# Kernel tuning notes

Hardware: AMD Instinct MI355X
Metric: run time of the kernel (lower is better)

The kernel has to match this reference:

```python
import jax, jax.numpy as jnp
import numpy as np

K = 51           # kernel_size
DENSE_INNER = 2
EPS_LN = 1e-6
EPS_GRN = 1e-6

def _make_peripheral_coords(radius, dense_inner=2):
    coords = list(range(0, min(radius, dense_inner) + 1))
    v = 1
    while v < radius:
        v *= 2
        if v > dense_inner and v < radius:
            coords.append(v)
    if radius not in coords:
        coords.append(radius)
    return sorted(set(coords))

def _quantise(a, coords):
    q = 0
    for c in coords:
        if c <= a:
            q = c
        else:
            break
    return q

def _build_idx_map(kernel_size, dense_inner):
    radius = kernel_size // 2
    coords = _make_peripheral_coords(radius, dense_inner)
    signed = [-c for c in reversed(coords[1:])] + list(coords)
    P = len(signed)
    c2i = {c: i for i, c in enumerate(signed)}
    idx = []
    for i in range(kernel_size):
        oi = i - radius
        qi = _quantise(abs(oi), coords)
        ii = c2i[-qi if oi < 0 else qi]
        for j in range(kernel_size):
            oj = j - radius
            qj = _quantise(abs(oj), coords)
            jj = c2i[-qj if oj < 0 else qj]
            idx.append(ii * P + jj)
    return np.asarray(idx, dtype=np.int32), P

IDX_MAP, P = _build_idx_map(K, DENSE_INNER)  # P == 13 for K=51

DIM = 384
HID = 4 * DIM

def setup_inputs() -> dict:
    key = jax.random.key(0)
    ks = jax.random.split(key, 10)
    B, C, H, W = 8, DIM, 64, 64
    std = 0.02
    return {
        "x": jax.random.normal(ks[0], (B, C, H, W), jnp.float32),
        "weight_comp": jax.random.normal(ks[1], (C, P * P), jnp.float32) * std,
        "kpe": jax.random.normal(ks[2], (1, 1, K, K), jnp.float32) * std,
        "ln_w": jnp.ones((C,), jnp.float32),
        "ln_b": jnp.zeros((C,), jnp.float32),
        "w1": jax.random.normal(ks[3], (C, HID), jnp.float32) * std,
        "b1": jnp.zeros((HID,), jnp.float32),
        "grn_gamma": jax.random.normal(ks[4], (HID,), jnp.float32) * std,
        "grn_beta": jax.random.normal(ks[5], (HID,), jnp.float32) * std,
        "w2": jax.random.normal(ks[6], (HID, C), jnp.float32) * std,
        "b2": jnp.zeros((C,), jnp.float32),
    }

def _block(x, weight_comp, kpe, ln_w, ln_b, w1, b1, grn_gamma, grn_beta, w2, b2):
    C = x.shape[1]
    # gather-built peripheral depthwise kernel: (C, 1, K, K) + shared positional bias
    w = weight_comp[:, IDX_MAP].reshape(C, 1, K, K) + kpe
    y = jax.lax.conv_general_dilated(
        x, w, window_strides=(1, 1), padding=[(K // 2, K // 2)] * 2,
        feature_group_count=C, dimension_numbers=("NCHW", "OIHW", "NCHW"))
    h = y.transpose(0, 2, 3, 1)  # NHWC
    # LayerNorm (channels_last, biased variance, eps=1e-6)
    mu = jnp.mean(h, axis=-1, keepdims=True)
    var = jnp.mean(jnp.square(h - mu), axis=-1, keepdims=True)
    h = (h - mu) * jax.lax.rsqrt(var + EPS_LN) * ln_w + ln_b
    # pointwise MLP with GRN
    h = jnp.einsum("nhwc,cf->nhwf", h, w1) + b1
    h = jax.nn.gelu(h, approximate=False)  # nn.GELU default is exact erf form
    gx = jnp.sqrt(jnp.sum(jnp.square(h), axis=(1, 2), keepdims=True))  # (N,1,1,F)
    nx = gx / (jnp.mean(gx, axis=-1, keepdims=True) + EPS_GRN)
    h = grn_gamma * (h * nx) + grn_beta + h
    h = jnp.einsum("nhwf,fc->nhwc", h, w2) + b2
    return x + h.transpose(0, 3, 1, 2)

def reference(x, weight_comp, kpe, ln_w, ln_b, w1, b1, grn_gamma, grn_beta, w2, b2):
    return _block(x, weight_comp, kpe, ln_w, ln_b, w1, b1, grn_gamma, grn_beta, w2, b2)
```

## Files before the change

kernel.cpp:

```cpp
#include <hip/hip_runtime.h>

#define CDIM 384
#define FDIM 1536
#define KK 51
#define RAD 25
#define NPIX 32768
#define HW 4096

#define CSTR 136
#define OSTR 68

typedef float  f32x4  __attribute__((ext_vector_type(4)));
typedef short  short8 __attribute__((ext_vector_type(8)));
typedef __bf16 bf16x8 __attribute__((ext_vector_type(8)));
typedef unsigned short us4 __attribute__((ext_vector_type(4)));

__device__ __constant__ int AXIS[51] = {
  0,
  1,1,1,1,1,1,1,1,1,
  2,2,2,2,2,2,2,2,
  3,3,3,3,
  4,4,
  5,
  6,
  7,
  8,8,
  9,9,9,9,
  10,10,10,10,10,10,10,10,
  11,11,11,11,11,11,11,11,11,
  12
};

__device__ __forceinline__ unsigned short bf16_rn(float x){
  union { float f; unsigned u; } v; v.f = x;
  unsigned r = v.u + 0x7FFFu + ((v.u >> 16) & 1u);
  return (unsigned short)(r >> 16);
}
__device__ __forceinline__ unsigned short f2bf(float x){
  __bf16 h = (__bf16)x;
  return __builtin_bit_cast(unsigned short, h);
}
__device__ __forceinline__ float bf2f(unsigned short h){
  union { unsigned u; float f; } v; v.u = ((unsigned)h) << 16; return v.f;
}
__device__ __forceinline__ float gelu_f(float v){
  float t = v*(0.7978845608f + 0.0356774081f*v*v);
  float sg = 1.f/(1.f + __expf(-2.f*t));
  return v * sg;
}

__global__ __launch_bounds__(256) void k_prep(const float* __restrict__ wc,
                                              const float* __restrict__ kpe,
                                              float* __restrict__ wfull,
                                              const float* __restrict__ w1,
                                              unsigned short* __restrict__ w1T,
                                              const float* __restrict__ w2,
                                              unsigned short* __restrict__ w2T,
                                              const float* __restrict__ beta,
                                              const float* __restrict__ b2,
                                              float* __restrict__ c2,
                                              float* __restrict__ grn){
  __shared__ float tile[64][65];
  __shared__ float red[256];
  int bid = blockIdx.x;
  int tid = threadIdx.x;
  if (bid < 384){
    int c = bid;
    const float* wcc = wc + c*169;
    float* wo = wfull + (size_t)c*2601;
    for (int idx = tid; idx < 2601; idx += 256){
      int i = idx / 51, j = idx - i*51;
      wo[idx] = wcc[AXIS[i]*13 + AXIS[j]] + kpe[idx];
    }
  } else if (bid < 672){
    const float* src; unsigned short* dst; int R, C, t;
    if (bid < 528){ src = w1; dst = w1T; R = CDIM; C = FDIM; t = bid - 384; }
    else          { src = w2; dst = w2T; R = FDIM; C = CDIM; t = bid - 528; }
    int nct = C >> 6;
    int tc = t % nct, tr = t / nct;
    int r0 = tr*64, c0 = tc*64;
    int lane = tid & 63, q = tid >> 6;
    #pragma unroll
    for (int it = 0; it < 16; ++it){
      int r = it*4 + q;
      tile[r][lane] = src[(size_t)(r0 + r)*C + c0 + lane];
    }
    __syncthreads();
    #pragma unroll
    for (int it = 0; it < 16; ++it){
      int c = it*4 + q;
      dst[(size_t)(c0 + c)*R + r0 + lane] = f2bf(tile[lane][c]);
    }
  } else if (bid < 678){
    int lane = tid & 63, w = tid >> 6;
    int c = (bid - 672)*64 + lane;
    float s = 0.f;
    for (int f = w*384; f < (w + 1)*384; ++f)
      s += beta[f] * w2[(size_t)f*CDIM + c];
    red[w*64 + lane] = s;
    __syncthreads();
    if (tid < 64){
      float t = red[tid] + red[64 + tid] + red[128 + tid] + red[192 + tid];
      c2[c] = t + b2[c];
    }
  } else {
    for (int i = tid; i < 8*FDIM; i += 256) grn[i] = 0.f;
  }
}

__global__ __launch_bounds__(256) void k_conv_mfma(const float* __restrict__ x,
                                                   const float* __restrict__ wfull,
                                                   float* __restrict__ y,
                                                   int img0){
  __shared__ __align__(16) float outb[64*OSTR];
  __shared__ __align__(16) unsigned short buf[4][1088];
  int img = img0 + blockIdx.x;
  int ch  = img % CDIM;
  const float* xim = x + (size_t)img*HW;
  const float* wch = wfull + (size_t)ch*2601;
  int tid = threadIdx.x;
  int lane = tid & 63, wid = tid >> 6;
  int li = lane & 15, g = lane >> 4;
  int t0 = (lane & 31) << 2;
  int c0 = lane >> 5;

  for (int i = tid; i < 1088; i += 256)
    *(f32x4*)&outb[i*4] = (f32x4){0.f,0.f,0.f,0.f};

  bf16x8 Bf[4][2];
  #pragma unroll
  for (int nt = 0; nt < 4; ++nt){
    int i = nt*16 + li;
    #pragma unroll
    for (int kt = 0; kt < 2; ++kt){
      union { bf16x8 v; unsigned short u[8]; } tmp;
      #pragma unroll
      for (int e = 0; e < 8; ++e){
        int j = kt*32 + g*8 + e;
        float v = (i < 51 && j < 51) ? wch[i*51 + j] : 0.f;
        tmp.u[e] = bf16_rn(v);
      }
      Bf[nt][kt] = tmp.v;
    }
  }

  {
    const float* xr = xim + (16*wid)*64;
    #pragma unroll
    for (int it = 0; it < 4; ++it){
      int c = c0 + 2*it;
      us4 o;
      #pragma unroll
      for (int e = 0; e < 4; ++e){
        int xi = t0 + e + c - 25;
        float v = (xi >= 0 && xi < 64) ? xr[xi] : 0.f;
        o[e] = bf16_rn(v);
      }
      *(us4*)&buf[wid][c*CSTR + t0] = o;
    }
  }
  __syncthreads();

  #pragma unroll 1
  for (int ph = 0; ph < 16; ++ph){
    float pf[16];
    if (ph + 1 < 16){
      const float* xr = xim + (ph + 1 + 16*wid)*64;
      #pragma unroll
      for (int it = 0; it < 4; ++it){
        int c = c0 + 2*it;
        #pragma unroll
        for (int e = 0; e < 4; ++e){
          int xi = t0 + e + c - 25;
          int xc = min(max(xi, 0), 63);
          pf[it*4 + e] = xr[xc];
        }
      }
    }

    bf16x8 Af[4][2];
    #pragma unroll
    for (int s = 0; s < 4; ++s){
      const unsigned short* bb = &buf[s][0];
      #pragma unroll
      for (int kt = 0; kt < 2; ++kt){
        int u0 = wid*16 + kt*32 + g*8 + li;
        int c  = li & 7;
        Af[s][kt] = *(const bf16x8*)&bb[c*CSTR + (u0 - c)];
      }
    }

    #pragma unroll
    for (int dd = 0; dd < 6; ++dd){
      int d = dd - 2;
      int pmax = ph + 25 + 16*d;
      if (pmax < 0 || pmax > 78) continue;
      f32x4 V = {0.f,0.f,0.f,0.f};
      #pragma unroll
      for (int s = 0; s < 4; ++s){
        int nt = s - d;
        if (nt < 0 || nt > 3) continue;
        V = __builtin_amdgcn_mfma_f32_16x16x32_bf16(Af[s][0], Bf[nt][0], V, 0, 0, 0);
        V = __builtin_amdgcn_mfma_f32_16x16x32_bf16(Af[s][1], Bf[nt][1], V, 0, 0, 0);
      }
      int p = pmax - li;
      if (p >= 0 && p < 64){
        float* oa = &outb[p*OSTR + wid*16 + g*4];
        f32x4 old = *(const f32x4*)oa;
        *(f32x4*)oa = old + V;
      }
    }

    __syncthreads();
    if (ph + 1 < 16){
      unsigned short* dst = &buf[wid][0];
      #pragma unroll
      for (int it = 0; it < 4; ++it){
        int c = c0 + 2*it;
        us4 o;
        #pragma unroll
        for (int e = 0; e < 4; ++e){
          int xi = t0 + e + c - 25;
          float v = (xi >= 0 && xi < 64) ? pf[it*4 + e] : 0.f;
          o[e] = bf16_rn(v);
        }
        *(us4*)&dst[c*CSTR + t0] = o;
      }
    }
    __syncthreads();
  }

  float* yo = y + (size_t)img*HW;
  #pragma unroll
  for (int k = 0; k < 4; ++k){
    int pix = k*1024 + tid*4;
    int p = pix >> 6, q = pix & 63;
    *(f32x4*)(yo + pix) = *(const f32x4*)&outb[p*OSTR + q];
  }
}

__global__ __launch_bounds__(256) void k_gemm1p(const float* __restrict__ y,
                                                const float* __restrict__ lnw,
                                                const float* __restrict__ lnb,
                                                const unsigned short* __restrict__ BT,
                                                const float* __restrict__ b1,
                                                unsigned short* __restrict__ H,
                                                float* __restrict__ grn){
  __shared__ __align__(16) unsigned short pan[64*392];
  __shared__ __align__(16) unsigned short bS[2][128*40];
  __shared__ float sred[2][4][64];
  int m0 = blockIdx.x * 64;
  int img = m0 >> 12;
  int tid = threadIdx.x;
  int lane = tid & 63, wid = tid >> 6;
  int wr = wid >> 1, wc = wid & 1;
  int lm = lane & 15, g = lane >> 4;
  int sr = tid & 127, sc = tid >> 7;

  {
    int sp0 = m0 & 4095;
    const float* yb = y + (size_t)img*CDIM*HW + sp0 + lane;
    int cbase = wid*96;
    float v[96];
    float sum = 0.f, sq = 0.f;
    #pragma unroll
    for (int cc = 0; cc < 96; ++cc){
      float t = yb[(size_t)(cbase + cc)*HW];
      v[cc] = t; sum += t; sq += t*t;
    }
    sred[0][wid][lane] = sum; sred[1][wid][lane] = sq;
    __syncthreads();
    float ts = 0.f, tq = 0.f;
    #pragma unroll
    for (int u = 0; u < 4; ++u){ ts += sred[0][u][lane]; tq += sred[1][u][lane]; }
    float mu   = ts * (1.f/CDIM);
    float rstd = rsqrtf(tq * (1.f/CDIM) - mu*mu + 1e-6f);
    #pragma unroll
    for (int j = 0; j < 12; ++j){
      short8 o;
      #pragma unroll
      for (int e = 0; e < 8; ++e){
        int c = cbase + j*8 + e;
        float t = (v[j*8 + e] - mu) * rstd * lnw[c] + lnb[c];
        o[e] = (short)f2bf(t);
      }
      *(short8*)&pan[lane*392 + cbase + j*8] = o;
    }
  }

  {
    const unsigned short* gb = BT + (size_t)sr*CDIM + sc*16;
    *(short8*)&bS[0][sr*40 + sc*16]     = *(const short8*)(gb);
    *(short8*)&bS[0][sr*40 + sc*16 + 8] = *(const short8*)(gb + 8);
  }
  short8 rn0, rn1;
  {
    const unsigned short* gb = BT + (size_t)sr*CDIM + 32 + sc*16;
    rn0 = *(const short8*)(gb);
    rn1 = *(const short8*)(gb + 8);
  }
  int pft = 0, pk = 64;
  int par = 0;

  #pragma unroll 1
  for (int ft = 0; ft < 12; ++ft){
    f32x4 acc[2][4];
    #pragma unroll
    for (int i = 0; i < 2; ++i)
      #pragma unroll
      for (int j = 0; j < 4; ++j) acc[i][j] = (f32x4){0.f,0.f,0.f,0.f};

    #pragma unroll 1
    for (int ks = 0; ks < 12; ++ks){
      int k0 = ks*32;
      __syncthreads();
      if (!(ft == 11 && ks == 11)){
        *(short8*)&bS[par^1][sr*40 + sc*16]     = rn0;
        *(short8*)&bS[par^1][sr*40 + sc*16 + 8] = rn1;
      }
      if (!(ft == 11 && ks >= 10)){
        const unsigned short* gb = BT + (size_t)(pft*128 + sr)*CDIM + pk + sc*16;
        rn0 = *(const short8*)(gb);
        rn1 = *(const short8*)(gb + 8);
        pk += 32; if (pk == CDIM){ pk = 0; ++pft; }
      }
      bf16x8 aF[2], bF[4];
      #pragma unroll
      for (int fm = 0; fm < 2; ++fm) aF[fm] = *(const bf16x8*)&pan[(wr*32 + fm*16 + lm)*392 + k0 + g*8];
      #pragma unroll
      for (int fn = 0; fn < 4; ++fn) bF[fn] = *(const bf16x8*)&bS[par][(wc*64 + fn*16 + lm)*40 + g*8];
      #pragma unroll
      for (int fm = 0; fm < 2; ++fm)
        #pragma unroll
        for (int fn = 0; fn < 4; ++fn)
          acc[fm][fn] = __builtin_amdgcn_mfma_f32_16x16x32_bf16(aF[fm], bF[fn], acc[fm][fn], 0, 0, 0);
      par ^= 1;
    }

    int n0 = ft*128;
    float psum[4] = {0.f,0.f,0.f,0.f};
    #pragma unroll
    for (int fn = 0; fn < 4; ++fn){
      int n = n0 + wc*64 + fn*16 + lm;
      float bias = b1[n];
      #pragma unroll
      for (int fm = 0; fm < 2; ++fm){
        int mb = m0 + wr*32 + fm*16 + g*4;
        #pragma unroll
        for (int r = 0; r < 4; ++r){
          float v = gelu_f(acc[fm][fn][r] + bias);
          H[(size_t)(mb + r)*FDIM + n] = f2bf(v);
          psum[fn] += v*v;
        }
      }
    }
    #pragma unroll
    for (int fn = 0; fn < 4; ++fn){
      float v = psum[fn];
      v += __shfl_xor(v, 16);
      v += __shfl_xor(v, 32);
      if (g == 0){
        atomicAdd(&grn[img*FDIM + n0 + wc*64 + fn*16 + lm], v);
      }
    }
  }
}

__global__ __launch_bounds__(256) void k_grn(const float* __restrict__ grn,
                                             const float* __restrict__ gamma,
                                             float* __restrict__ S){
  int n = blockIdx.x;
  const float* g = grn + n*FDIM;
  __shared__ float red[256];
  float p = 0.f;
  for (int f = threadIdx.x; f < FDIM; f += 256) p += sqrtf(g[f]);
  red[threadIdx.x] = p;
  __syncthreads();
  for (int s = 128; s > 0; s >>= 1){
    if (threadIdx.x < s) red[threadIdx.x] += red[threadIdx.x + s];
    __syncthreads();
  }
  float mean = red[0] * (1.f/FDIM);
  float inv = 1.f/(mean + 1e-6f);
  for (int f = threadIdx.x; f < FDIM; f += 256){
    float nx = sqrtf(g[f]) * inv;
    S[n*FDIM + f] = 1.f + gamma[f]*nx;
  }
}

__global__ __launch_bounds__(256) void k_scale(const unsigned short* __restrict__ w2T,
                                               const float* __restrict__ S,
                                               unsigned short* __restrict__ W2s){
  int img = blockIdx.y;
  size_t base = ((size_t)blockIdx.x*256 + threadIdx.x)*8;
  int f0 = (int)(base % FDIM);
  const float* Si = S + img*FDIM + f0;
  short8 wv = *(const short8*)(w2T + base);
  short8 o;
  #pragma unroll
  for (int e = 0; e < 8; ++e)
    o[e] = (short)f2bf(bf2f((unsigned short)wv[e]) * Si[e]);
  *(short8*)(W2s + (size_t)img*CDIM*FDIM + base) = o;
}

__global__ __launch_bounds__(256) void k_gemm2(const unsigned short* __restrict__ W2s,
                                               const unsigned short* __restrict__ H,
                                               const float* __restrict__ c2,
                                               const float* __restrict__ xg,
                                               float* __restrict__ out){
  __shared__ __align__(16) unsigned short aS[2][128*40];
  __shared__ __align__(16) unsigned short bS[2][128*40];
  int bid = blockIdx.x;
  int x8 = bid & 7;
  int kk = bid >> 3;
  int bm = kk % 3;
  int bn = x8 + 8*(kk / 3);
  int c0 = bm*128, p0 = bn*128;
  int img = p0 >> 12;
  const unsigned short* Wimg = W2s + (size_t)img*CDIM*FDIM;
  int tid = threadIdx.x;
  int lane = tid & 63, wid = tid >> 6;
  int wr = wid >> 1, wc = wid & 1;
  int lm = lane & 15, g = lane >> 4;
  int sr = tid & 127, sc = tid >> 7;
  f32x4 acc[4][4];
  #pragma unroll
  for (int i = 0; i < 4; ++i)
    #pragma unroll
    for (int j = 0; j < 4; ++j) acc[i][j] = (f32x4){0.f,0.f,0.f,0.f};

  {
    const unsigned short* ga = Wimg + (size_t)(c0 + sr)*FDIM + sc*16;
    *(short8*)&aS[0][sr*40 + sc*16]     = *(const short8*)(ga);
    *(short8*)&aS[0][sr*40 + sc*16 + 8] = *(const short8*)(ga + 8);
    const unsigned short* gb = H + (size_t)(p0 + sr)*FDIM + sc*16;
    *(short8*)&bS[0][sr*40 + sc*16]     = *(const short8*)(gb);
    *(short8*)&bS[0][sr*40 + sc*16 + 8] = *(const short8*)(gb + 8);
  }
  short8 ra0, ra1, rh0, rh1;
  {
    const unsigned short* ga = Wimg + (size_t)(c0 + sr)*FDIM + 32 + sc*16;
    ra0 = *(const short8*)(ga); ra1 = *(const short8*)(ga + 8);
    const unsigned short* gb = H + (size_t)(p0 + sr)*FDIM + 32 + sc*16;
    rh0 = *(const short8*)(gb); rh1 = *(const short8*)(gb + 8);
  }
  int par = 0;

  #pragma unroll 1
  for (int ks = 0; ks < 48; ++ks){
    __syncthreads();
    if (ks + 1 < 48){
      *(short8*)&aS[par^1][sr*40 + sc*16]     = ra0;
      *(short8*)&aS[par^1][sr*40 + sc*16 + 8] = ra1;
      *(short8*)&bS[par^1][sr*40 + sc*16]     = rh0;
      *(short8*)&bS[par^1][sr*40 + sc*16 + 8] = rh1;
    }
    if (ks + 2 < 48){
      int nk = (ks + 2)*32;
      const unsigned short* ga = Wimg + (size_t)(c0 + sr)*FDIM + nk + sc*16;
      ra0 = *(const short8*)(ga); ra1 = *(const short8*)(ga + 8);
      const unsigned short* gb = H + (size_t)(p0 + sr)*FDIM + nk + sc*16;
      rh0 = *(const short8*)(gb); rh1 = *(const short8*)(gb + 8);
    }
    bf16x8 aF[4], bF[4];
    #pragma unroll
    for (int fm = 0; fm < 4; ++fm) aF[fm] = *(const bf16x8*)&aS[par][(wr*64 + fm*16 + lm)*40 + g*8];
    #pragma unroll
    for (int fn = 0; fn < 4; ++fn) bF[fn] = *(const bf16x8*)&bS[par][(wc*64 + fn*16 + lm)*40 + g*8];
    #pragma unroll
    for (int fm = 0; fm < 4; ++fm)
      #pragma unroll
      for (int fn = 0; fn < 4; ++fn)
        acc[fm][fn] = __builtin_amdgcn_mfma_f32_16x16x32_bf16(aF[fm], bF[fn], acc[fm][fn], 0, 0, 0);
    par ^= 1;
  }

  int sp0 = p0 & 4095;
  #pragma unroll
  for (int fn = 0; fn < 4; ++fn){
    int pixoff = sp0 + wc*64 + fn*16 + lm;
    #pragma unroll
    for (int fm = 0; fm < 4; ++fm){
      #pragma unroll
      for (int r = 0; r < 4; ++r){
        int c = c0 + wr*64 + fm*16 + g*4 + r;
        size_t addr = ((size_t)img*CDIM + c)*HW + pixoff;
        out[addr] = acc[fm][fn][r] + c2[c] + xg[addr];
      }
    }
  }
}

extern "C" void kernel_launch(void* const* d_in, const int* in_sizes, int n_in,
                              void* d_out, int out_size, void* d_ws, size_t ws_size,
                              hipStream_t stream) {
  const float* x    = (const float*)d_in[0];
  const float* wc   = (const float*)d_in[1];
  const float* kpe  = (const float*)d_in[2];
  const float* lnw  = (const float*)d_in[3];
  const float* lnb  = (const float*)d_in[4];
  const float* w1   = (const float*)d_in[5];
  const float* b1   = (const float*)d_in[6];
  const float* gam  = (const float*)d_in[7];
  const float* beta = (const float*)d_in[8];
  const float* w2   = (const float*)d_in[9];
  const float* b2   = (const float*)d_in[10];
  float* out = (float*)d_out;

  char* ws = (char*)d_ws;
  size_t o = 0;
  auto take = [&](size_t bytes)->char*{
    char* p = ws + o;
    o = (o + bytes + 511) & ~(size_t)511;
    return p;
  };
  float*          y     = out;
  float*          wfull = (float*)take((size_t)CDIM*2601*4);
  unsigned short* H     = (unsigned short*)take((size_t)NPIX*FDIM*2);
  unsigned short* w1T   = (unsigned short*)take((size_t)CDIM*FDIM*2);
  unsigned short* w2T   = (unsigned short*)take((size_t)CDIM*FDIM*2);
  unsigned short* W2s   = (unsigned short*)take((size_t)8*CDIM*FDIM*2);
  float*          grn   = (float*)take(8*FDIM*4);
  float*          S     = (float*)take(8*FDIM*4);
  float*          c2    = (float*)take(CDIM*4);
  if (o > ws_size) return;

  k_prep<<<679, 256, 0, stream>>>(wc, kpe, wfull, w1, w1T, w2, w2T, beta, b2, c2, grn);
  k_conv_mfma<<<1536, 256, 0, stream>>>(x, wfull, y, 0);
  k_conv_mfma<<<1536, 256, 0, stream>>>(x, wfull, y, 1536);
  k_gemm1p<<<NPIX/64, 256, 0, stream>>>(y, lnw, lnb, w1T, b1, H, grn);
  k_grn<<<8, 256, 0, stream>>>(grn, gam, S);
  k_scale<<<dim3(288, 8), 256, 0, stream>>>(w2T, S, W2s);
  k_gemm2<<<3*(NPIX/128), 256, 0, stream>>>(W2s, H, c2, x, out);
}
```

Measured before the change: 382.2 us.

## Retile GEMM1 into 128x128 output tiles with streamed LayerNorm A-operand

Replaces the panel GEMM, where each block held 64 pixels' full LayerNormed row and looped over all 12 feature tiles, with a 2D-tiled kernel over 3072 blocks of 128 pixels by 128 features. Each block computes LayerNorm stats with a first pass over y, then normalizes and converts A slices per K-step, double-buffered in LDS alongside B, with register prefetch two steps ahead. Block IDs are swizzled so 8 adjacent pixel tiles share a feature tile, aiming for L2 reuse of the weights. This increases parallelism and MFMA work per LDS load, but each block rereads y twice and the stats pass is recomputed for all 12 feature tiles.

```diff
diff --git a/kernel.cpp b/kernel.cpp
--- a/kernel.cpp
+++ b/kernel.cpp
@@ -239,129 +239,138 @@
   }
 }
 
-__global__ __launch_bounds__(256) void k_gemm1p(const float* __restrict__ y,
+__global__ __launch_bounds__(256) void k_gemm1t(const float* __restrict__ y,
                                                 const float* __restrict__ lnw,
                                                 const float* __restrict__ lnb,
                                                 const unsigned short* __restrict__ BT,
                                                 const float* __restrict__ b1,
                                                 unsigned short* __restrict__ H,
                                                 float* __restrict__ grn){
-  __shared__ __align__(16) unsigned short pan[64*392];
+  __shared__ __align__(16) unsigned short aS[2][128*40];
   __shared__ __align__(16) unsigned short bS[2][128*40];
-  __shared__ float sred[2][4][64];
-  int m0 = blockIdx.x * 64;
-  int img = m0 >> 12;
+  __shared__ float sred[2][2][128];
+  int bid = blockIdx.x;
+  int x8 = bid & 7;
+  int kk = bid >> 3;
+  int bm = kk % 12;
+  int bn = x8 + 8*(kk/12);
+  int p0 = bn*128, n0 = bm*128;
+  int img = p0 >> 12;
+  int sp0 = p0 & 4095;
   int tid = threadIdx.x;
   int lane = tid & 63, wid = tid >> 6;
   int wr = wid >> 1, wc = wid & 1;
   int lm = lane & 15, g = lane >> 4;
+  int px = tid & 127, hh = tid >> 7;
   int sr = tid & 127, sc = tid >> 7;
 
-  {
-    int sp0 = m0 & 4095;
-    const float* yb = y + (size_t)img*CDIM*HW + sp0 + lane;
-    int cbase = wid*96;
-    float v[96];
+  const float* yb = y + (size_t)img*CDIM*HW + sp0 + px;
+  {
     float sum = 0.f, sq = 0.f;
-    #pragma unroll
-    for (int cc = 0; cc < 96; ++cc){
-      float t = yb[(size_t)(cbase + cc)*HW];
-      v[cc] = t; sum += t; sq += t*t;
-    }
-    sred[0][wid][lane] = sum; sred[1][wid][lane] = sq;
-    __syncthreads();
-    float ts = 0.f, tq = 0.f;
-    #pragma unroll
-    for (int u = 0; u < 4; ++u){ ts += sred[0][u][lane]; tq += sred[1][u][lane]; }
-    float mu   = ts * (1.f/CDIM);
-    float rstd = rsqrtf(tq * (1.f/CDIM) - mu*mu + 1e-6f);
-    #pragma unroll
-    for (int j = 0; j < 12; ++j){
-      short8 o;
-      #pragma unroll
-      for (int e = 0; e < 8; ++e){
-        int c = cbase + j*8 + e;
-        float t = (v[j*8 + e] - mu) * rstd * lnw[c] + lnb[c];
-        o[e] = (short)f2bf(t);
-      }
-      *(short8*)&pan[lane*392 + cbase + j*8] = o;
-    }
-  }
-
-  {
-    const unsigned short* gb = BT + (size_t)sr*CDIM + sc*16;
+    for (int c = hh*192; c < hh*192 + 192; ++c){
+      float v = yb[(size_t)c*HW];
+      sum += v; sq += v*v;
+    }
+    sred[hh][0][px] = sum; sred[hh][1][px] = sq;
+  }
+  __syncthreads();
+  float mu, rstd;
+  {
+    float ts = sred[0][0][px] + sred[1][0][px];
+    float tq = sred[0][1][px] + sred[1][1][px];
+    mu   = ts * (1.f/CDIM);
+    rstd = rsqrtf(tq * (1.f/CDIM) - mu*mu + 1e-6f);
+  }
+
+  {
+    short8 o0, o1;
+    #pragma unroll
+    for (int e = 0; e < 8; ++e){
+      int c = hh*16 + e;
+      o0[e] = (short)f2bf((yb[(size_t)c*HW] - mu)*rstd*lnw[c] + lnb[c]);
+      int c2_ = hh*16 + 8 + e;
+      o1[e] = (short)f2bf((yb[(size_t)c2_*HW] - mu)*rstd*lnw[c2_] + lnb[c2_]);
+    }
+    *(short8*)&aS[0][px*40 + hh*16]     = o0;
+    *(short8*)&aS[0][px*40 + hh*16 + 8] = o1;
+    const unsigned short* gb = BT + (size_t)(n0 + sr)*CDIM + sc*16;
     *(short8*)&bS[0][sr*40 + sc*16]     = *(const short8*)(gb);
     *(short8*)&bS[0][sr*40 + sc*16 + 8] = *(const short8*)(gb + 8);
   }
-  short8 rn0, rn1;
-  {
-    const unsigned short* gb = BT + (size_t)sr*CDIM + 32 + sc*16;
-    rn0 = *(const short8*)(gb);
-    rn1 = *(const short8*)(gb + 8);
-  }
-  int pft = 0, pk = 64;
+  float apre[16];
+  short8 bpre0, bpre1;
+  {
+    #pragma unroll
+    for (int e = 0; e < 16; ++e) apre[e] = yb[(size_t)(32 + hh*16 + e)*HW];
+    const unsigned short* gb = BT + (size_t)(n0 + sr)*CDIM + 32 + sc*16;
+    bpre0 = *(const short8*)(gb); bpre1 = *(const short8*)(gb + 8);
+  }
   int par = 0;
+  f32x4 acc[4][4];
+  #pragma unroll
+  for (int i = 0; i < 4; ++i)
+    #pragma unroll
+    for (int j = 0; j < 4; ++j) acc[i][j] = (f32x4){0.f,0.f,0.f,0.f};
 
   #pragma unroll 1
-  for (int ft = 0; ft < 12; ++ft){
-    f32x4 acc[2][4];
-    #pragma unroll
-    for (int i = 0; i < 2; ++i)
-      #pragma unroll
-      for (int j = 0; j < 4; ++j) acc[i][j] = (f32x4){0.f,0.f,0.f,0.f};
-
-    #pragma unroll 1
-    for (int ks = 0; ks < 12; ++ks){
-      int k0 = ks*32;
-      __syncthreads();
-      if (!(ft == 11 && ks == 11)){
-        *(short8*)&bS[par^1][sr*40 + sc*16]     = rn0;
-        *(short8*)&bS[par^1][sr*40 + sc*16 + 8] = rn1;
-      }
-      if (!(ft == 11 && ks >= 10)){
-        const unsigned short* gb = BT + (size_t)(pft*128 + sr)*CDIM + pk + sc*16;
-        rn0 = *(const short8*)(gb);
-        rn1 = *(const short8*)(gb + 8);
-        pk += 32; if (pk == CDIM){ pk = 0; ++pft; }
-      }
-      bf16x8 aF[2], bF[4];
-      #pragma unroll
-      for (int fm = 0; fm < 2; ++fm) aF[fm] = *(const bf16x8*)&pan[(wr*32 + fm*16 + lm)*392 + k0 + g*8];
-      #pragma unroll
-      for (int fn = 0; fn < 4; ++fn) bF[fn] = *(const bf16x8*)&bS[par][(wc*64 + fn*16 + lm)*40 + g*8];
-      #pragma unroll
-      for (int fm = 0; fm < 2; ++fm)
-        #pragma unroll
-        for (int fn = 0; fn < 4; ++fn)
-          acc[fm][fn] = __builtin_amdgcn_mfma_f32_16x16x32_bf16(aF[fm], bF[fn], acc[fm][fn], 0, 0, 0);
-      par ^= 1;
-    }
-
-    int n0 = ft*128;
-    float psum[4] = {0.f,0.f,0.f,0.f};
-    #pragma unroll
-    for (int fn = 0; fn < 4; ++fn){
-      int n = n0 + wc*64 + fn*16 + lm;
-      float bias = b1[n];
-      #pragma unroll
-      for (int fm = 0; fm < 2; ++fm){
-        int mb = m0 + wr*32 + fm*16 + g*4;
-        #pragma unroll
-        for (int r = 0; r < 4; ++r){
-          float v = gelu_f(acc[fm][fn][r] + bias);
-          H[(size_t)(mb + r)*FDIM + n] = f2bf(v);
-          psum[fn] += v*v;
-        }
-      }
-    }
-    #pragma unroll
-    for (int fn = 0; fn < 4; ++fn){
-      float v = psum[fn];
-      v += __shfl_xor(v, 16);
-      v += __shfl_xor(v, 32);
-      if (g == 0){
-        atomicAdd(&grn[img*FDIM + n0 + wc*64 + fn*16 + lm], v);
-      }
+  for (int ks = 0; ks < 12; ++ks){
+    __syncthreads();
+    if (ks + 1 < 12){
+      int ck = (ks + 1)*32 + hh*16;
+      short8 o0, o1;
+      #pragma unroll
+      for (int e = 0; e < 8; ++e){
+        o0[e] = (short)f2bf((apre[e]     - mu)*rstd*lnw[ck + e]     + lnb[ck + e]);
+        o1[e] = (short)f2bf((apre[8 + e] - mu)*rstd*lnw[ck + 8 + e] + lnb[ck + 8 + e]);
+      }
+      *(short8*)&aS[par^1][px*40 + hh*16]     = o0;
+      *(short8*)&aS[par^1][px*40 + hh*16 + 8] = o1;
+      *(short8*)&bS[par^1][sr*40 + sc*16]     = bpre0;
+      *(short8*)&bS[par^1][sr*40 + sc*16 + 8] = bpre1;
+    }
+    if (ks + 2 < 12){
+      int ck = (ks + 2)*32;
+      #pragma unroll
+      for (int e = 0; e < 16; ++e) apre[e] = yb[(size_t)(ck + hh*16 + e)*HW];
+      const unsigned short* gb = BT + (size_t)(n0 + sr)*CDIM + ck + sc*16;
+      bpre0 = *(const short8*)(gb); bpre1 = *(const short8*)(gb + 8);
+    }
+    bf16x8 aF[4], bF[4];
+    #pragma unroll
+    for (int fm = 0; fm < 4; ++fm) aF[fm] = *(const bf16x8*)&aS[par][(wr*64 + fm*16 + lm)*40 + g*8];
+    #pragma unroll
+    for (int fn = 0; fn < 4; ++fn) bF[fn] = *(const bf16x8*)&bS[par][(wc*64 + fn*16 + lm)*40 + g*8];
+    #pragma unroll
+    for (int fm = 0; fm < 4; ++fm)
+      #pragma unroll
+      for (int fn = 0; fn < 4; ++fn)
+        acc[fm][fn] = __builtin_amdgcn_mfma_f32_16x16x32_bf16(aF[fm], bF[fn], acc[fm][fn], 0, 0, 0);
+    par ^= 1;
+  }
+
+  float psum[4] = {0.f,0.f,0.f,0.f};
+  #pragma unroll
+  for (int fn = 0; fn < 4; ++fn){
+    int n = n0 + wc*64 + fn*16 + lm;
+    float bias = b1[n];
+    #pragma unroll
+    for (int fm = 0; fm < 4; ++fm){
+      int mb = p0 + wr*64 + fm*16 + g*4;
+      #pragma unroll
+      for (int r = 0; r < 4; ++r){
+        float v = gelu_f(acc[fm][fn][r] + bias);
+        H[(size_t)(mb + r)*FDIM + n] = f2bf(v);
+        psum[fn] += v*v;
+      }
+    }
+  }
+  #pragma unroll
+  for (int fn = 0; fn < 4; ++fn){
+    float v = psum[fn];
+    v += __shfl_xor(v, 16);
+    v += __shfl_xor(v, 32);
+    if (g == 0){
+      atomicAdd(&grn[img*FDIM + n0 + wc*64 + fn*16 + lm], v);
     }
   }
 }
@@ -528,7 +537,7 @@
   k_prep<<<679, 256, 0, stream>>>(wc, kpe, wfull, w1, w1T, w2, w2T, beta, b2, c2, grn);
   k_conv_mfma<<<1536, 256, 0, stream>>>(x, wfull, y, 0);
   k_conv_mfma<<<1536, 256, 0, stream>>>(x, wfull, y, 1536);
-  k_gemm1p<<<NPIX/64, 256, 0, stream>>>(y, lnw, lnb, w1T, b1, H, grn);
+  k_gemm1t<<<3072, 256, 0, stream>>>(y, lnw, lnb, w1T, b1, H, grn);
   k_grn<<<8, 256, 0, stream>>>(grn, gam, S);
   k_scale<<<dim3(288, 8), 256, 0, stream>>>(w2T, S, W2s);
   k_gemm2<<<3*(NPIX/128), 256, 0, stream>>>(W2s, H, c2, x, out);
```

After: 436.0 us. 1.14x slower.
